# Optimization experiments

Measured on AMD Instinct MI355X. Metric: run time of the kernel, lower is better.

The kernel has to match this reference:

```python
import jax, jax.numpy as jnp
import numpy as np

# YOLOv1 loss constants (from init_kwargs)
S, B, C = 28, 2, 20
L_COORD, L_NOOBJ = 5.0, 0.5
LEN_PRED = 5 * B + C  # 30
BS = 512


def setup_inputs() -> dict:
    key = jax.random.key(0)
    k1, k2, k3 = jax.random.split(key, 3)
    prediction = jax.random.uniform(k1, (BS, S, S, LEN_PRED), dtype=jnp.float32)
    target = jax.random.uniform(k2, (BS, S, S, LEN_PRED), dtype=jnp.float32)
    obj = jax.random.bernoulli(k3, 0.05, (BS, S, S)).astype(jnp.float32)
    idx = jnp.arange(LEN_PRED)
    is_conf = (idx < 5 * B) & (idx % 5 == 4)
    target = jnp.where(is_conf, obj[..., None], target)
    return {"prediction": prediction, "target": target}


def _xyxy(box):
    # [x, y, w, h] (cell-relative center, image-relative wh) -> [x1, y1, x2, y2]
    xy = box[..., :2] / S
    wh = box[..., 2:4]
    return xy - 0.5 * wh, xy + 0.5 * wh


def reference(prediction, target):
    N = prediction.shape[0]
    dt = prediction.dtype
    coo = (target[..., 4] > 0).astype(dt)   # (bs,S,S) cells with an object
    noo = 1.0 - coo                          # cells without an object

    pb = prediction[..., :5 * B].reshape(prediction.shape[:3] + (B, 5))  # (bs,S,S,B,5)
    tb = target[..., :5 * B].reshape(target.shape[:3] + (B, 5))

    # IoU of each predicted box vs the (single) target box of the cell
    p_lt, p_rb = _xyxy(pb)                 # (bs,S,S,B,2)
    t_lt, t_rb = _xyxy(tb[..., 0, :])      # (bs,S,S,2)
    lt = jnp.maximum(p_lt, t_lt[..., None, :])
    rb = jnp.minimum(p_rb, t_rb[..., None, :])
    wh = jnp.clip(rb - lt, 0.0)
    inter = wh[..., 0] * wh[..., 1]        # (bs,S,S,B)
    area1 = jnp.prod(p_rb - p_lt, axis=-1)
    area2 = jnp.prod(t_rb - t_lt, axis=-1)[..., None]
    iou = jax.lax.stop_gradient(inter / (area1 + area2 - inter))  # .data in torch

    max_idx = jnp.argmax(iou, axis=-1)     # responsible box per cell
    max_iou = jnp.max(iou, axis=-1)
    resp = jax.nn.one_hot(max_idx, B, dtype=dt)    # (bs,S,S,B)
    w_resp = coo[..., None] * resp                  # responsible & object
    w_not = coo[..., None] * (1.0 - resp)           # not responsible & object

    # Term 1+2: location loss (xy MSE + sqrt-wh MSE) on responsible boxes
    d_xy = jnp.sum((pb[..., :2] - tb[..., :2]) ** 2, axis=-1)
    d_wh = jnp.sum((jnp.sqrt(pb[..., 2:4]) - jnp.sqrt(tb[..., 2:4])) ** 2, axis=-1)
    loc_loss = jnp.sum(w_resp * (d_xy + d_wh))

    contain_loss = jnp.sum(w_resp * (pb[..., 4] - max_iou[..., None]) ** 2)

    # Term 4a: not-responsible boxes in object cells -> confidence target 0
    not_response_loss = jnp.sum(w_not * pb[..., 4] ** 2)

    # Term 4b: confidence loss in no-object cells (all B boxes)
    nooobj_loss = jnp.sum(noo[..., None] * (pb[..., 4] - tb[..., 4]) ** 2)

    # Term 5: class MSE in object cells
    class_loss = jnp.sum(coo[..., None] * (prediction[..., 5 * B:] - target[..., 5 * B:]) ** 2)

    loss = (L_COORD * loc_loss + contain_loss
            + L_NOOBJ * (not_response_loss + nooobj_loss) + class_loss)
    return loss / N
```

## Files before the change

kernel.cpp:

```cpp
#include <hip/hip_runtime.h>

namespace {
constexpr int   kCells      = 512 * 28 * 28;
constexpr int   kTPB        = 256;
constexpr int   kTileCells  = 256;
constexpr int   kTileF      = kTileCells * 30;
constexpr int   kWaveF      = 64 * 30;
constexpr int   kNBlocks    = kCells / kTileCells;
constexpr int   kNPart      = kNBlocks * 4;
constexpr float kLCoord     = 5.0f;
constexpr float kLNoobj     = 0.5f;
constexpr float kInvS       = 1.0f / 28.0f;
constexpr float kInvN       = 1.0f / 512.0f;
}

__device__ __forceinline__ void async16(const float* g, float* l) {
    __builtin_amdgcn_global_load_lds(
        (const __attribute__((address_space(1))) void*)g,
        (__attribute__((address_space(3))) void*)l,
        16, 0, 0);
}
__device__ __forceinline__ void async4(const float* g, float* l) {
    __builtin_amdgcn_global_load_lds(
        (const __attribute__((address_space(1))) void*)g,
        (__attribute__((address_space(3))) void*)l,
        4, 0, 0);
}

__device__ __forceinline__ float cell_loss(const float* p, const float* t) {
    const float coo = (t[4] > 0.0f) ? 1.0f : 0.0f;

    const float t_cx = t[0] * kInvS, t_cy = t[1] * kInvS;
    const float t_ltx = t_cx - 0.5f * t[2];
    const float t_lty = t_cy - 0.5f * t[3];
    const float t_rbx = t_cx + 0.5f * t[2];
    const float t_rby = t_cy + 0.5f * t[3];
    const float area2 = (t_rbx - t_ltx) * (t_rby - t_lty);

    float iou0 = 0.0f, iou1 = 0.0f;
    #pragma unroll
    for (int b = 0; b < 2; ++b) {
        const float* pb = p + 5 * b;
        const float p_cx = pb[0] * kInvS, p_cy = pb[1] * kInvS;
        const float p_ltx = p_cx - 0.5f * pb[2];
        const float p_lty = p_cy - 0.5f * pb[3];
        const float p_rbx = p_cx + 0.5f * pb[2];
        const float p_rby = p_cy + 0.5f * pb[3];
        const float ltx = fmaxf(p_ltx, t_ltx);
        const float lty = fmaxf(p_lty, t_lty);
        const float rbx = fminf(p_rbx, t_rbx);
        const float rby = fminf(p_rby, t_rby);
        const float w = fmaxf(rbx - ltx, 0.0f);
        const float h = fmaxf(rby - lty, 0.0f);
        const float inter = w * h;
        const float area1 = (p_rbx - p_ltx) * (p_rby - p_lty);
        const float iou = inter / (area1 + area2 - inter);
        if (b == 0) iou0 = iou; else iou1 = iou;
    }
    const int   max_idx = (iou1 > iou0) ? 1 : 0;
    const float max_iou = fmaxf(iou0, iou1);

    float loc = 0.0f, contain = 0.0f, notresp = 0.0f, nooobj = 0.0f;
    #pragma unroll
    for (int b = 0; b < 2; ++b) {
        const float* pb = p + 5 * b;
        const float* tb = t + 5 * b;
        const float dx = pb[0] - tb[0];
        const float dy = pb[1] - tb[1];
        const float d_xy = dx * dx + dy * dy;
        const float sw = sqrtf(pb[2]) - sqrtf(tb[2]);
        const float sh = sqrtf(pb[3]) - sqrtf(tb[3]);
        const float d_wh = sw * sw + sh * sh;
        const float resp   = (b == max_idx) ? 1.0f : 0.0f;
        const float w_resp = coo * resp;
        const float w_not  = coo * (1.0f - resp);
        loc += w_resp * (d_xy + d_wh);
        const float dc = pb[4] - max_iou;
        contain += w_resp * dc * dc;
        notresp += w_not * pb[4] * pb[4];
        const float dn = pb[4] - tb[4];
        nooobj += (1.0f - coo) * dn * dn;
    }

    float cls = 0.0f;
    #pragma unroll
    for (int j = 10; j < 30; ++j) {
        const float d = p[j] - t[j];
        cls += d * d;
    }
    cls *= coo;

    return kLCoord * loc + contain + kLNoobj * (notresp + nooobj) + cls;
}

template <bool USE_WS>
__global__ __launch_bounds__(kTPB) void yolo_loss_kernel(
        const float* __restrict__ pred,
        const float* __restrict__ targ,
        float* __restrict__ dst) {
    __shared__ float lp[kTileF];
    __shared__ float lt[kTileF];

    const int tid  = threadIdx.x;
    const int lane = tid & 63;
    const int wid  = tid >> 6;

    const float* gp = pred + (size_t)blockIdx.x * kTileF + wid * kWaveF;
    const float* gt = targ + (size_t)blockIdx.x * kTileF + wid * kWaveF;
    float* wlp = &lp[wid * kWaveF];
    float* wlt = &lt[wid * kWaveF];

    #pragma unroll
    for (int c = 0; c < 7; ++c) {
        const int f = c * 256 + lane * 4;
        async16(gp + f, wlp + c * 256);
        async16(gt + f, wlt + c * 256);
    }
    #pragma unroll
    for (int c = 0; c < 2; ++c) {
        const int f = 1792 + c * 64 + lane;
        async4(gp + f, wlp + 1792 + c * 64);
        async4(gt + f, wlt + 1792 + c * 64);
    }
    asm volatile("s_waitcnt vmcnt(0)" ::: "memory");

    float local = cell_loss(&lp[tid * 30], &lt[tid * 30]);

    #pragma unroll
    for (int off = 32; off > 0; off >>= 1)
        local += __shfl_down(local, off, 64);

    if (lane == 0) {
        if (USE_WS) dst[blockIdx.x * 4 + wid] = local;
        else        atomicAdd(dst, local * kInvN);
    }
}

__global__ __launch_bounds__(256) void reduce_kernel(
        const float* __restrict__ part, float* __restrict__ out) {
    __shared__ float wsum[4];
    float s = 0.0f;
    for (int i = threadIdx.x; i < kNPart; i += 256) s += part[i];
    #pragma unroll
    for (int off = 32; off > 0; off >>= 1)
        s += __shfl_down(s, off, 64);
    const int lane = threadIdx.x & 63;
    const int wid  = threadIdx.x >> 6;
    if (lane == 0) wsum[wid] = s;
    __syncthreads();
    if (threadIdx.x == 0)
        out[0] = (wsum[0] + wsum[1] + wsum[2] + wsum[3]) * kInvN;
}

__global__ void zero_out_kernel(float* __restrict__ out) {
    if (threadIdx.x == 0) out[0] = 0.0f;
}

extern "C" void kernel_launch(void* const* d_in, const int* in_sizes, int n_in,
                              void* d_out, int out_size, void* d_ws, size_t ws_size,
                              hipStream_t stream) {
    const float* pred = (const float*)d_in[0];
    const float* targ = (const float*)d_in[1];
    float* out = (float*)d_out;

    if (ws_size >= (size_t)kNPart * sizeof(float)) {
        float* part = (float*)d_ws;
        yolo_loss_kernel<true><<<kNBlocks, kTPB, 0, stream>>>(pred, targ, part);
        reduce_kernel<<<1, 256, 0, stream>>>(part, out);
    } else {
        zero_out_kernel<<<1, 64, 0, stream>>>(out);
        yolo_loss_kernel<false><<<kNBlocks, kTPB, 0, stream>>>(pred, targ, out);
    }
}
```

Measured before the change: 28.07 us.

## Switch to persistent single-wave blocks with double-buffered async LDS loads

Replaces the one-tile-per-256-thread-block launch with 1280 persistent 64-thread blocks. Each block strides over 64-cell tiles and double-buffers global-to-LDS async loads, waiting with a partial vmcnt so the next tile's load overlaps the current tile's compute. The partial-sum count drops from 6272 to 1280, which shortens the final reduction. In exchange, each wave holds only two tiles in flight, and with fewer waves per CU there may be less memory-level parallelism than in the original oversubscribed launch.

```diff
diff --git a/kernel.cpp b/kernel.cpp
--- a/kernel.cpp
+++ b/kernel.cpp
@@ -1,17 +1,15 @@
 #include <hip/hip_runtime.h>
 
 namespace {
-constexpr int   kCells      = 512 * 28 * 28;
-constexpr int   kTPB        = 256;
-constexpr int   kTileCells  = 256;
-constexpr int   kTileF      = kTileCells * 30;
-constexpr int   kWaveF      = 64 * 30;
-constexpr int   kNBlocks    = kCells / kTileCells;
-constexpr int   kNPart      = kNBlocks * 4;
-constexpr float kLCoord     = 5.0f;
-constexpr float kLNoobj     = 0.5f;
-constexpr float kInvS       = 1.0f / 28.0f;
-constexpr float kInvN       = 1.0f / 512.0f;
+constexpr int   kCells     = 512 * 28 * 28;
+constexpr int   kTileCells = 64;
+constexpr int   kNTiles    = kCells / kTileCells;
+constexpr int   kWaveF     = kTileCells * 30;
+constexpr int   kNWaves    = 1280;
+constexpr float kLCoord    = 5.0f;
+constexpr float kLNoobj    = 0.5f;
+constexpr float kInvS      = 1.0f / 28.0f;
+constexpr float kInvN      = 1.0f / 512.0f;
 }
 
 __device__ __forceinline__ void async16(const float* g, float* l) {
@@ -94,45 +92,60 @@
 }
 
 template <bool USE_WS>
-__global__ __launch_bounds__(kTPB) void yolo_loss_kernel(
+__global__ __launch_bounds__(64) void yolo_loss_kernel(
         const float* __restrict__ pred,
         const float* __restrict__ targ,
         float* __restrict__ dst) {
-    __shared__ float lp[kTileF];
-    __shared__ float lt[kTileF];
+    __shared__ float lp[2][kWaveF];
+    __shared__ float lt[2][kWaveF];
 
-    const int tid  = threadIdx.x;
-    const int lane = tid & 63;
-    const int wid  = tid >> 6;
+    const int lane = threadIdx.x;
+    const int w    = blockIdx.x;
 
-    const float* gp = pred + (size_t)blockIdx.x * kTileF + wid * kWaveF;
-    const float* gt = targ + (size_t)blockIdx.x * kTileF + wid * kWaveF;
-    float* wlp = &lp[wid * kWaveF];
-    float* wlt = &lt[wid * kWaveF];
+    const int T = 1 + (kNTiles - 1 - w) / kNWaves;
 
-    #pragma unroll
-    for (int c = 0; c < 7; ++c) {
-        const int f = c * 256 + lane * 4;
-        async16(gp + f, wlp + c * 256);
-        async16(gt + f, wlt + c * 256);
+    auto stage = [&](int tile, int buf) {
+        const float* gp = pred + (size_t)tile * kWaveF;
+        const float* gt = targ + (size_t)tile * kWaveF;
+        #pragma unroll
+        for (int c = 0; c < 7; ++c) {
+            const int f = c * 256 + lane * 4;
+            async16(gp + f, &lp[buf][c * 256]);
+            async16(gt + f, &lt[buf][c * 256]);
+        }
+        #pragma unroll
+        for (int c = 0; c < 2; ++c) {
+            const int f = 1792 + c * 64 + lane;
+            async4(gp + f, &lp[buf][1792 + c * 64]);
+            async4(gt + f, &lt[buf][1792 + c * 64]);
+        }
+    };
+
+    stage(w, 0);
+    if (T > 1) stage(w + kNWaves, 1);
+
+    float acc = 0.0f;
+    for (int i = 0; i < T; ++i) {
+        const int cur = i & 1;
+        if (i + 1 < T) {
+            asm volatile("s_waitcnt vmcnt(18)" ::: "memory");
+        } else {
+            asm volatile("s_waitcnt vmcnt(0)" ::: "memory");
+        }
+        acc += cell_loss(&lp[cur][lane * 30], &lt[cur][lane * 30]);
+        if (i + 2 < T) {
+            asm volatile("s_waitcnt lgkmcnt(0)" ::: "memory");
+            stage(w + (i + 2) * kNWaves, cur);
+        }
     }
-    #pragma unroll
-    for (int c = 0; c < 2; ++c) {
-        const int f = 1792 + c * 64 + lane;
-        async4(gp + f, wlp + 1792 + c * 64);
-        async4(gt + f, wlt + 1792 + c * 64);
-    }
-    asm volatile("s_waitcnt vmcnt(0)" ::: "memory");
-
-    float local = cell_loss(&lp[tid * 30], &lt[tid * 30]);
 
     #pragma unroll
     for (int off = 32; off > 0; off >>= 1)
-        local += __shfl_down(local, off, 64);
+        acc += __shfl_down(acc, off, 64);
 
     if (lane == 0) {
-        if (USE_WS) dst[blockIdx.x * 4 + wid] = local;
-        else        atomicAdd(dst, local * kInvN);
+        if (USE_WS) dst[w] = acc;
+        else        atomicAdd(dst, acc * kInvN);
     }
 }
 
@@ -140,7 +153,7 @@
         const float* __restrict__ part, float* __restrict__ out) {
     __shared__ float wsum[4];
     float s = 0.0f;
-    for (int i = threadIdx.x; i < kNPart; i += 256) s += part[i];
+    for (int i = threadIdx.x; i < kNWaves; i += 256) s += part[i];
     #pragma unroll
     for (int off = 32; off > 0; off >>= 1)
         s += __shfl_down(s, off, 64);
@@ -163,12 +176,12 @@
     const float* targ = (const float*)d_in[1];
     float* out = (float*)d_out;
 
-    if (ws_size >= (size_t)kNPart * sizeof(float)) {
+    if (ws_size >= (size_t)kNWaves * sizeof(float)) {
         float* part = (float*)d_ws;
-        yolo_loss_kernel<true><<<kNBlocks, kTPB, 0, stream>>>(pred, targ, part);
+        yolo_loss_kernel<true><<<kNWaves, 64, 0, stream>>>(pred, targ, part);
         reduce_kernel<<<1, 256, 0, stream>>>(part, out);
     } else {
         zero_out_kernel<<<1, 64, 0, stream>>>(out);
-        yolo_loss_kernel<false><<<kNBlocks, kTPB, 0, stream>>>(pred, targ, out);
+        yolo_loss_kernel<false><<<kNWaves, 64, 0, stream>>>(pred, targ, out);
     }
 }
```

After: 24.78 us. 11.7% less time.
